# Kernel tuning notes

Measured on AMD Instinct MI355X. Metric: run time of the kernel, lower is better.

## Reference

```python
import jax, jax.numpy as jnp
import numpy as np

D_MODEL, D_FF, N_EXPERTS, TOP_K = 1024, 4096, 8, 2
B, S = 4, 1024
EPS = 1e-5

def setup_inputs() -> dict:
    key = jax.random.key(0)
    ks = jax.random.split(key, 8)
    sd = 1.0 / np.sqrt(D_MODEL)
    sf = 1.0 / np.sqrt(D_FF)
    return {
        "x": jax.random.normal(ks[0], (B, S, D_MODEL), dtype=jnp.float32),
        "mask": jnp.ones((B, S), dtype=bool),
        "Wg": jax.random.normal(ks[1], (D_MODEL, N_EXPERTS), dtype=jnp.float32) * sd,
        "W1": jax.random.normal(ks[2], (N_EXPERTS, D_MODEL, D_FF), dtype=jnp.float32) * sd,
        "b1": jnp.zeros((N_EXPERTS, D_FF), dtype=jnp.float32),
        "W2": jax.random.normal(ks[3], (N_EXPERTS, D_FF, D_MODEL), dtype=jnp.float32) * sf,
        "b2": jnp.zeros((N_EXPERTS, D_MODEL), dtype=jnp.float32),
        "gamma": jnp.ones((D_MODEL,), dtype=jnp.float32),
        "beta": jnp.zeros((D_MODEL,), dtype=jnp.float32),
    }

def _layernorm(x, gamma, beta):
    mu = jnp.mean(x, axis=-1, keepdims=True)
    var = jnp.mean(jnp.square(x - mu), axis=-1, keepdims=True)
    return (x - mu) * jax.lax.rsqrt(var + EPS) * gamma + beta

def reference(x, mask, Wg, W1, b1, W2, b2, gamma, beta):
    Bq, Sq, D = x.shape
    T = Bq * Sq
    xf = x.reshape(T, D)                       # [T, D]
    logits = xf @ Wg                           # [T, E]
    probs = jax.nn.softmax(logits, axis=-1)
    topv, topi = jax.lax.top_k(probs, TOP_K)   # [T, K]
    w = topv / jnp.sum(topv, axis=-1, keepdims=True)
    combine = jnp.zeros((T, N_EXPERTS), dtype=probs.dtype)
    combine = combine.at[jnp.arange(T)[:, None], topi].add(w)  # [T, E]
    # all-expert FFN (dense reference for grouped expert GEMMs)
    h = jax.nn.relu(jnp.einsum('td,edf->tef', xf, W1) + b1)    # [T, E, F]
    ye = jnp.einsum('tef,efd->ted', h, W2) + b2                # [T, E, D]
    y = jnp.einsum('te,ted->td', combine, ye)                  # [T, D]
    # load-balancing aux loss (Switch-style)
    frac_tokens = jnp.mean((combine > 0).astype(probs.dtype), axis=0)  # [E]
    frac_probs = jnp.mean(probs, axis=0)                                # [E]
    aux_loss = N_EXPERTS * jnp.sum(frac_tokens * frac_probs)
    out = _layernorm(x + y.reshape(Bq, Sq, D), gamma, beta)
    return out, aux_loss
```

## Files before the change

### kernel.cpp

```cpp
#include <hip/hip_runtime.h>
#include <cstdint>
#include <cstddef>


#define T_TOK 4096
#define DM 1024
#define DF 4096
#define NE 8
#define CAP 9216
#define MAXMT 72

typedef __bf16 bf16;
typedef __bf16 bf16x4 __attribute__((ext_vector_type(4)));
typedef __bf16 bf16x8 __attribute__((ext_vector_type(8)));
typedef float f32x4 __attribute__((ext_vector_type(4)));

struct Meta {
  int pad_off[NE + 1];
  int n_mtiles;
  int tile_e[80];
  int tile_m0[80];
};

__global__ __launch_bounds__(256) void router_kernel(
    const float* __restrict__ x, const float* __restrict__ Wg,
    int* __restrict__ topi, float* __restrict__ topw, float* __restrict__ probs) {
  int wave = threadIdx.x >> 6, lane = threadIdx.x & 63;
  int t = blockIdx.x * 4 + wave;
  const float* xr = x + (size_t)t * DM;
  float acc[NE];
#pragma unroll
  for (int e = 0; e < NE; e++) acc[e] = 0.f;
  for (int d0 = 0; d0 < DM; d0 += 64) {
    float xv = xr[d0 + lane];
    const float4* wrow = (const float4*)(Wg + (size_t)(d0 + lane) * NE);
    float4 w0 = wrow[0], w1 = wrow[1];
    acc[0] += xv * w0.x; acc[1] += xv * w0.y; acc[2] += xv * w0.z; acc[3] += xv * w0.w;
    acc[4] += xv * w1.x; acc[5] += xv * w1.y; acc[6] += xv * w1.z; acc[7] += xv * w1.w;
  }
#pragma unroll
  for (int off = 32; off >= 1; off >>= 1) {
#pragma unroll
    for (int e = 0; e < NE; e++) acc[e] += __shfl_xor(acc[e], off);
  }
  if (lane == 0) {
    float m = acc[0];
#pragma unroll
    for (int e = 1; e < NE; e++) m = fmaxf(m, acc[e]);
    float p[NE], s = 0.f;
#pragma unroll
    for (int e = 0; e < NE; e++) { p[e] = expf(acc[e] - m); s += p[e]; }
    float inv = 1.f / s;
#pragma unroll
    for (int e = 0; e < NE; e++) { p[e] *= inv; probs[t * NE + e] = p[e]; }
    int i1 = 0; float v1 = acc[0];
#pragma unroll
    for (int e = 1; e < NE; e++) if (acc[e] > v1) { v1 = acc[e]; i1 = e; }
    int i2 = -1; float v2 = -1e30f;
#pragma unroll
    for (int e = 0; e < NE; e++) if (e != i1 && acc[e] > v2) { v2 = acc[e]; i2 = e; }
    float sw = p[i1] + p[i2];
    topi[t * 2] = i1; topi[t * 2 + 1] = i2;
    topw[t * 2] = p[i1] / sw; topw[t * 2 + 1] = p[i2] / sw;
  }
}

__global__ __launch_bounds__(256) void prep_kernel(
    const int* __restrict__ topi, const float* __restrict__ probs,
    Meta* __restrict__ meta, float* __restrict__ aux_out) {
  __shared__ int scnt[NE];
  __shared__ float wps[4][NE];
  int tid = threadIdx.x, lane = tid & 63, wave = tid >> 6;
  if (tid < NE) scnt[tid] = 0;
  __syncthreads();
  for (int i = tid; i < T_TOK * 2; i += 256) atomicAdd(&scnt[topi[i]], 1);
  float lp[NE];
#pragma unroll
  for (int e = 0; e < NE; e++) lp[e] = 0.f;
  for (int tt = tid; tt < T_TOK; tt += 256) {
#pragma unroll
    for (int e = 0; e < NE; e++) lp[e] += probs[tt * NE + e];
  }
#pragma unroll
  for (int off = 32; off >= 1; off >>= 1) {
#pragma unroll
    for (int e = 0; e < NE; e++) lp[e] += __shfl_xor(lp[e], off);
  }
  if (lane == 0) {
#pragma unroll
    for (int e = 0; e < NE; e++) wps[wave][e] = lp[e];
  }
  __syncthreads();
  if (tid == 0) {
    float aux = 0.f;
    int nt = 0, po = 0;
    for (int e = 0; e < NE; e++) {
      float ps = wps[0][e] + wps[1][e] + wps[2][e] + wps[3][e];
      aux += (float)scnt[e] * ps;
      meta->pad_off[e] = po;
      int pc = (scnt[e] + 127) & ~127;
      for (int i = 0; i < pc / 128; i++) {
        meta->tile_e[nt] = e; meta->tile_m0[nt] = po + i * 128; nt++;
      }
      po += pc;
    }
    meta->pad_off[NE] = po;
    meta->n_mtiles = nt;
    aux_out[0] = aux * (8.f / ((float)T_TOK * (float)T_TOK));
  }
}

__global__ __launch_bounds__(64) void scatter_kernel(
    const int* __restrict__ topi, const float* __restrict__ topw,
    const Meta* __restrict__ meta,
    int* __restrict__ t_of, float* __restrict__ w_of, int* __restrict__ k_of) {
  int e = blockIdx.x, lane = threadIdx.x;
  int base = meta->pad_off[e];
  for (int c = 0; c < T_TOK * 2; c += 64) {
    int idx = c + lane;
    int sel = (topi[idx] == e) ? 1 : 0;
    unsigned long long mask = __ballot(sel);
    if (sel) {
      int rank = __popcll(mask & ((1ull << lane) - 1ull));
      int s = base + rank;
      t_of[s] = idx >> 1;
      k_of[s] = idx & 1;
      w_of[s] = topw[idx];
    }
    base += (int)__popcll(mask);
  }
}

__global__ __launch_bounds__(256) void gather_kernel(
    const float* __restrict__ x, const int* __restrict__ t_of,
    unsigned short* __restrict__ Xg_u) {
  int s = blockIdx.x;
  int t = t_of[s];
  if (t < 0) return;
  bf16* Xg = (bf16*)Xg_u;
  int i = threadIdx.x;
  float4 v = ((const float4*)(x + (size_t)t * DM))[i];
  bf16x4 o = {(bf16)v.x, (bf16)v.y, (bf16)v.z, (bf16)v.w};
  ((bf16x4*)(Xg + (size_t)s * DM))[i] = o;
}

__global__ __launch_bounds__(256) void transpose_kernel(
    const float* __restrict__ src, unsigned short* __restrict__ dst_u, int R, int C) {
  bf16* dst = (bf16*)dst_u;
  int e = blockIdx.z;
  int c0 = blockIdx.x * 32, r0 = blockIdx.y * 32;
  int tx = threadIdx.x & 31, ty = threadIdx.x >> 5;
  __shared__ float tile[32][33];
  const float* s = src + (size_t)e * R * C;
#pragma unroll
  for (int j = 0; j < 32; j += 8)
    tile[ty + j][tx] = s[(size_t)(r0 + ty + j) * C + c0 + tx];
  __syncthreads();
  bf16* d = dst + (size_t)e * C * R;
#pragma unroll
  for (int j = 0; j < 32; j += 8)
    d[(size_t)(c0 + ty + j) * R + r0 + tx] = (bf16)tile[tx][ty + j];
}

__device__ inline void gl_lds16(const void* g, void* l) {
  __builtin_amdgcn_global_load_lds(
      (const __attribute__((address_space(1))) unsigned int*)g,
      (__attribute__((address_space(3))) unsigned int*)l, 16, 0, 0);
}

template <int MODE>
__global__ __launch_bounds__(256) void gemm_kernel(
    const unsigned short* __restrict__ A_u, const unsigned short* __restrict__ Bt_u,
    const float* __restrict__ bias, const Meta* __restrict__ meta,
    int K, int N,
    unsigned short* __restrict__ Hout_u, float* __restrict__ Yout,
    const int* __restrict__ t_of, const int* __restrict__ k_of,
    const float* __restrict__ w_of) {
  int bx = blockIdx.x;
  if (bx >= meta->n_mtiles) return;
  const bf16* A = (const bf16*)A_u;
  const bf16* Bt = (const bf16*)Bt_u;
  int e = meta->tile_e[bx];
  int m0 = meta->tile_m0[bx];
  int n0 = blockIdx.y * 128;
  const bf16* Be = Bt + (size_t)e * N * K;

  __shared__ bf16 As[128 * 64];
  __shared__ bf16 Bs[128 * 64];

  int tid = threadIdx.x, lane = tid & 63, wave = tid >> 6;
  int wr = wave >> 1, wc = wave & 1;
  int srow = lane >> 3;
  int scol = (lane & 7) * 8;

  const bf16* Ag = A + (size_t)(m0 + wave * 8 + srow) * K + scol;
  const bf16* Bg = Be + (size_t)(n0 + wave * 8 + srow) * K + scol;
  bf16* AsW = As + wave * 512;
  bf16* BsW = Bs + wave * 512;

  f32x4 acc[4][4];
#pragma unroll
  for (int i = 0; i < 4; i++)
#pragma unroll
    for (int j = 0; j < 4; j++) acc[i][j] = (f32x4){0.f, 0.f, 0.f, 0.f};

  int fr = lane & 15;
  int kq = (lane >> 4) * 8;

  for (int k0 = 0; k0 < K; k0 += 64) {
#pragma unroll
    for (int r = 0; r < 4; r++) {
      gl_lds16(Ag + (size_t)(r * 32) * K + k0, AsW + r * 2048);
      gl_lds16(Bg + (size_t)(r * 32) * K + k0, BsW + r * 2048);
    }
    __syncthreads();
#pragma unroll
    for (int kk = 0; kk < 64; kk += 32) {
      bf16x8 af[4], bfr[4];
#pragma unroll
      for (int i = 0; i < 4; i++)
        af[i] = *(const bf16x8*)&As[(wr * 64 + i * 16 + fr) * 64 + kk + kq];
#pragma unroll
      for (int j = 0; j < 4; j++)
        bfr[j] = *(const bf16x8*)&Bs[(wc * 64 + j * 16 + fr) * 64 + kk + kq];
#pragma unroll
      for (int i = 0; i < 4; i++)
#pragma unroll
        for (int j = 0; j < 4; j++)
          acc[i][j] = __builtin_amdgcn_mfma_f32_16x16x32_bf16(af[i], bfr[j], acc[i][j], 0, 0, 0);
    }
    __syncthreads();
  }

  int crow = (lane >> 4) * 4;
  int ccol = lane & 15;
  if (MODE == 1) {
    bf16* Hout = (bf16*)Hout_u;
#pragma unroll
    for (int i = 0; i < 4; i++) {
#pragma unroll
      for (int r = 0; r < 4; r++) {
        int slot = m0 + wr * 64 + i * 16 + crow + r;
        bf16* hrow = Hout + (size_t)slot * N;
#pragma unroll
        for (int j = 0; j < 4; j++) {
          int n = n0 + wc * 64 + j * 16 + ccol;
          float v = acc[i][j][r] + bias[e * N + n];
          hrow[n] = (bf16)fmaxf(v, 0.f);
        }
      }
    }
  } else {
#pragma unroll
    for (int i = 0; i < 4; i++) {
#pragma unroll
      for (int r = 0; r < 4; r++) {
        int slot = m0 + wr * 64 + i * 16 + crow + r;
        int t = t_of[slot];
        if (t < 0) continue;
        int ks = k_of[slot];
        float w = w_of[slot];
        float* yrow = Yout + ((size_t)ks * T_TOK + t) * DM;
#pragma unroll
        for (int j = 0; j < 4; j++) {
          int n = n0 + wc * 64 + j * 16 + ccol;
          yrow[n] = (acc[i][j][r] + bias[e * DM + n]) * w;
        }
      }
    }
  }
}

__global__ __launch_bounds__(256) void ln_kernel(
    const float* __restrict__ x, const float* __restrict__ Ysl,
    const float* __restrict__ gamma, const float* __restrict__ beta,
    float* __restrict__ out) {
  int t = blockIdx.x, tid = threadIdx.x, lane = tid & 63, wave = tid >> 6;
  float4 a = ((const float4*)(x + (size_t)t * DM))[tid];
  float4 y0 = ((const float4*)(Ysl + (size_t)t * DM))[tid];
  float4 y1 = ((const float4*)(Ysl + ((size_t)T_TOK + t) * DM))[tid];
  float4 sv;
  sv.x = a.x + y0.x + y1.x; sv.y = a.y + y0.y + y1.y;
  sv.z = a.z + y0.z + y1.z; sv.w = a.w + y0.w + y1.w;
  float sum = sv.x + sv.y + sv.z + sv.w;
  float sq = sv.x * sv.x + sv.y * sv.y + sv.z * sv.z + sv.w * sv.w;
#pragma unroll
  for (int off = 32; off >= 1; off >>= 1) {
    sum += __shfl_xor(sum, off);
    sq += __shfl_xor(sq, off);
  }
  __shared__ float ls[4], lq[4], stats[2];
  if (lane == 0) { ls[wave] = sum; lq[wave] = sq; }
  __syncthreads();
  if (tid == 0) {
    float ts = ls[0] + ls[1] + ls[2] + ls[3];
    float tq = lq[0] + lq[1] + lq[2] + lq[3];
    float mu = ts * (1.f / DM);
    float var = tq * (1.f / DM) - mu * mu;
    stats[0] = mu;
    stats[1] = rsqrtf(var + 1e-5f);
  }
  __syncthreads();
  float mu = stats[0], rs = stats[1];
  float4 g = ((const float4*)gamma)[tid];
  float4 b = ((const float4*)beta)[tid];
  float4 o;
  o.x = (sv.x - mu) * rs * g.x + b.x;
  o.y = (sv.y - mu) * rs * g.y + b.y;
  o.z = (sv.z - mu) * rs * g.z + b.z;
  o.w = (sv.w - mu) * rs * g.w + b.w;
  ((float4*)(out + (size_t)t * DM))[tid] = o;
}

extern "C" void kernel_launch(void* const* d_in, const int* in_sizes, int n_in,
                              void* d_out, int out_size, void* d_ws, size_t ws_size,
                              hipStream_t stream) {
  const float* x     = (const float*)d_in[0];
  const float* Wg    = (const float*)d_in[2];
  const float* W1    = (const float*)d_in[3];
  const float* b1    = (const float*)d_in[4];
  const float* W2    = (const float*)d_in[5];
  const float* b2    = (const float*)d_in[6];
  const float* gamma = (const float*)d_in[7];
  const float* beta  = (const float*)d_in[8];
  float* out = (float*)d_out;

  char* ws = (char*)d_ws;
  size_t off = 0;
  auto alloc = [&](size_t bytes) -> void* {
    off = (off + 4095) & ~(size_t)4095;
    void* p = ws + off;
    off += bytes;
    return p;
  };
  Meta* meta   = (Meta*)alloc(sizeof(Meta));
  int* topi    = (int*)alloc((size_t)T_TOK * 2 * 4);
  float* topw  = (float*)alloc((size_t)T_TOK * 2 * 4);
  float* probs = (float*)alloc((size_t)T_TOK * NE * 4);
  int* t_of    = (int*)alloc((size_t)CAP * 4);
  int* k_of    = (int*)alloc((size_t)CAP * 4);
  float* w_of  = (float*)alloc((size_t)CAP * 4);
  unsigned short* Xg   = (unsigned short*)alloc((size_t)CAP * DM * 2);
  unsigned short* Hbuf = (unsigned short*)alloc((size_t)CAP * DF * 2);
  float* Ysl           = (float*)alloc((size_t)2 * T_TOK * DM * 4);
  unsigned short* WT   = (unsigned short*)alloc((size_t)NE * DM * DF * 2);

  hipMemsetAsync(t_of, 0xFF, (size_t)CAP * 4, stream);

  router_kernel<<<dim3(T_TOK / 4), dim3(256), 0, stream>>>(x, Wg, topi, topw, probs);
  prep_kernel<<<dim3(1), dim3(256), 0, stream>>>(topi, probs, meta, out + (size_t)T_TOK * DM);
  scatter_kernel<<<dim3(NE), dim3(64), 0, stream>>>(topi, topw, meta, t_of, w_of, k_of);
  gather_kernel<<<dim3(CAP), dim3(256), 0, stream>>>(x, t_of, Xg);

  transpose_kernel<<<dim3(DF / 32, DM / 32, NE), dim3(256), 0, stream>>>(W1, WT, DM, DF);
  gemm_kernel<1><<<dim3(MAXMT, DF / 128), dim3(256), 0, stream>>>(
      Xg, WT, b1, meta, DM, DF, Hbuf, (float*)nullptr,
      (const int*)nullptr, (const int*)nullptr, (const float*)nullptr);

  transpose_kernel<<<dim3(DM / 32, DF / 32, NE), dim3(256), 0, stream>>>(W2, WT, DF, DM);
  gemm_kernel<2><<<dim3(MAXMT, DM / 128), dim3(256), 0, stream>>>(
      Hbuf, WT, b2, meta, DF, DM, (unsigned short*)nullptr, Ysl, t_of, k_of, w_of);

  ln_kernel<<<dim3(T_TOK), dim3(256), 0, stream>>>(x, Ysl, gamma, beta, out);
}
```

Measured before the change: 751.1 us.

## Split-K second expert GEMM, swizzle LDS tiles, vectorize transpose stores

The second expert GEMM now splits K in two over a new grid z dimension. Each half writes its partial sums to a separate buffer, one of which reuses the Xg region, and the layernorm kernel adds the four partial slices. Both GEMMs also XOR-swizzle the 16-byte granules in LDS, both on global-to-LDS load and on fragment read, to cut bank conflicts. The weight transpose writes bf16 pairs instead of single elements. The split doubles the parallelism of the narrow N=1024 GEMM at the cost of extra fp32 partial-sum traffic to write and read back in layernorm.

```diff
diff --git a/kernel.cpp b/kernel.cpp
--- a/kernel.cpp
+++ b/kernel.cpp
@@ -11,6 +11,7 @@
 #define MAXMT 72
 
 typedef __bf16 bf16;
+typedef __bf16 bf16x2 __attribute__((ext_vector_type(2)));
 typedef __bf16 bf16x4 __attribute__((ext_vector_type(4)));
 typedef __bf16 bf16x8 __attribute__((ext_vector_type(8)));
 typedef float f32x4 __attribute__((ext_vector_type(4)));
@@ -157,9 +158,14 @@
     tile[ty + j][tx] = s[(size_t)(r0 + ty + j) * C + c0 + tx];
   __syncthreads();
   bf16* d = dst + (size_t)e * C * R;
-#pragma unroll
-  for (int j = 0; j < 32; j += 8)
-    d[(size_t)(c0 + ty + j) * R + r0 + tx] = (bf16)tile[tx][ty + j];
+  int wr_ = threadIdx.x & 15;
+  int wc_ = threadIdx.x >> 4;
+#pragma unroll
+  for (int j = 0; j < 32; j += 16) {
+    int c = wc_ + j;
+    bf16x2 v = {(bf16)tile[2 * wr_][c], (bf16)tile[2 * wr_ + 1][c]};
+    *(bf16x2*)&d[(size_t)(c0 + c) * R + r0 + 2 * wr_] = v;
+  }
 }
 
 __device__ inline void gl_lds16(const void* g, void* l) {
@@ -172,8 +178,9 @@
 __global__ __launch_bounds__(256) void gemm_kernel(
     const unsigned short* __restrict__ A_u, const unsigned short* __restrict__ Bt_u,
     const float* __restrict__ bias, const Meta* __restrict__ meta,
-    int K, int N,
-    unsigned short* __restrict__ Hout_u, float* __restrict__ Yout,
+    int Ktot, int Ksp, int N,
+    unsigned short* __restrict__ Hout_u,
+    float* __restrict__ P0, float* __restrict__ P1,
     const int* __restrict__ t_of, const int* __restrict__ k_of,
     const float* __restrict__ w_of) {
   int bx = blockIdx.x;
@@ -183,7 +190,8 @@
   int e = meta->tile_e[bx];
   int m0 = meta->tile_m0[bx];
   int n0 = blockIdx.y * 128;
-  const bf16* Be = Bt + (size_t)e * N * K;
+  int koff = blockIdx.z * Ksp;
+  const bf16* Be = Bt + (size_t)e * N * Ktot;
 
   __shared__ bf16 As[128 * 64];
   __shared__ bf16 Bs[128 * 64];
@@ -191,10 +199,11 @@
   int tid = threadIdx.x, lane = tid & 63, wave = tid >> 6;
   int wr = wave >> 1, wc = wave & 1;
   int srow = lane >> 3;
-  int scol = (lane & 7) * 8;
-
-  const bf16* Ag = A + (size_t)(m0 + wave * 8 + srow) * K + scol;
-  const bf16* Bg = Be + (size_t)(n0 + wave * 8 + srow) * K + scol;
+  int sgran = lane & 7;
+  int gcol = (sgran ^ srow) * 8;
+
+  const bf16* Ag = A + (size_t)(m0 + wave * 8 + srow) * Ktot + koff + gcol;
+  const bf16* Bg = Be + (size_t)(n0 + wave * 8 + srow) * Ktot + koff + gcol;
   bf16* AsW = As + wave * 512;
   bf16* BsW = Bs + wave * 512;
 
@@ -205,24 +214,26 @@
     for (int j = 0; j < 4; j++) acc[i][j] = (f32x4){0.f, 0.f, 0.f, 0.f};
 
   int fr = lane & 15;
-  int kq = (lane >> 4) * 8;
-
-  for (int k0 = 0; k0 < K; k0 += 64) {
+  int qh = lane >> 4;
+  int swz = fr & 7;
+
+  for (int k0 = 0; k0 < Ksp; k0 += 64) {
 #pragma unroll
     for (int r = 0; r < 4; r++) {
-      gl_lds16(Ag + (size_t)(r * 32) * K + k0, AsW + r * 2048);
-      gl_lds16(Bg + (size_t)(r * 32) * K + k0, BsW + r * 2048);
+      gl_lds16(Ag + (size_t)(r * 32) * Ktot + k0, AsW + r * 2048);
+      gl_lds16(Bg + (size_t)(r * 32) * Ktot + k0, BsW + r * 2048);
     }
     __syncthreads();
 #pragma unroll
     for (int kk = 0; kk < 64; kk += 32) {
+      int col = (((kk >> 3) | qh) ^ swz) * 8;
       bf16x8 af[4], bfr[4];
 #pragma unroll
       for (int i = 0; i < 4; i++)
-        af[i] = *(const bf16x8*)&As[(wr * 64 + i * 16 + fr) * 64 + kk + kq];
+        af[i] = *(const bf16x8*)&As[(wr * 64 + i * 16 + fr) * 64 + col];
 #pragma unroll
       for (int j = 0; j < 4; j++)
-        bfr[j] = *(const bf16x8*)&Bs[(wc * 64 + j * 16 + fr) * 64 + kk + kq];
+        bfr[j] = *(const bf16x8*)&Bs[(wc * 64 + j * 16 + fr) * 64 + col];
 #pragma unroll
       for (int i = 0; i < 4; i++)
 #pragma unroll
@@ -251,6 +262,8 @@
       }
     }
   } else {
+    float* Pz = (blockIdx.z == 0) ? P0 : P1;
+    int addb = (blockIdx.z == 0) ? 1 : 0;
 #pragma unroll
     for (int i = 0; i < 4; i++) {
 #pragma unroll
@@ -260,11 +273,12 @@
         if (t < 0) continue;
         int ks = k_of[slot];
         float w = w_of[slot];
-        float* yrow = Yout + ((size_t)ks * T_TOK + t) * DM;
+        float* yrow = Pz + ((size_t)ks * T_TOK + t) * DM;
 #pragma unroll
         for (int j = 0; j < 4; j++) {
           int n = n0 + wc * 64 + j * 16 + ccol;
-          yrow[n] = (acc[i][j][r] + bias[e * DM + n]) * w;
+          float bv = addb ? bias[e * DM + n] : 0.f;
+          yrow[n] = (acc[i][j][r] + bv) * w;
         }
       }
     }
@@ -272,16 +286,23 @@
 }
 
 __global__ __launch_bounds__(256) void ln_kernel(
-    const float* __restrict__ x, const float* __restrict__ Ysl,
+    const float* __restrict__ x,
+    const float* __restrict__ P0, const float* __restrict__ P1,
     const float* __restrict__ gamma, const float* __restrict__ beta,
     float* __restrict__ out) {
   int t = blockIdx.x, tid = threadIdx.x, lane = tid & 63, wave = tid >> 6;
-  float4 a = ((const float4*)(x + (size_t)t * DM))[tid];
-  float4 y0 = ((const float4*)(Ysl + (size_t)t * DM))[tid];
-  float4 y1 = ((const float4*)(Ysl + ((size_t)T_TOK + t) * DM))[tid];
+  size_t row = (size_t)t * DM;
+  size_t kstride = (size_t)T_TOK * DM;
+  float4 a  = ((const float4*)(x + row))[tid];
+  float4 y0 = ((const float4*)(P0 + row))[tid];
+  float4 y1 = ((const float4*)(P0 + kstride + row))[tid];
+  float4 y2 = ((const float4*)(P1 + row))[tid];
+  float4 y3 = ((const float4*)(P1 + kstride + row))[tid];
   float4 sv;
-  sv.x = a.x + y0.x + y1.x; sv.y = a.y + y0.y + y1.y;
-  sv.z = a.z + y0.z + y1.z; sv.w = a.w + y0.w + y1.w;
+  sv.x = a.x + y0.x + y1.x + y2.x + y3.x;
+  sv.y = a.y + y0.y + y1.y + y2.y + y3.y;
+  sv.z = a.z + y0.z + y1.z + y2.z + y3.z;
+  sv.w = a.w + y0.w + y1.w + y2.w + y3.w;
   float sum = sv.x + sv.y + sv.z + sv.w;
   float sq = sv.x * sv.x + sv.y * sv.y + sv.z * sv.z + sv.w * sv.w;
 #pragma unroll
@@ -309,7 +330,7 @@
   o.y = (sv.y - mu) * rs * g.y + b.y;
   o.z = (sv.z - mu) * rs * g.z + b.z;
   o.w = (sv.w - mu) * rs * g.w + b.w;
-  ((float4*)(out + (size_t)t * DM))[tid] = o;
+  ((float4*)(out + row))[tid] = o;
 }
 
 extern "C" void kernel_launch(void* const* d_in, const int* in_sizes, int n_in,
@@ -340,9 +361,13 @@
   int* t_of    = (int*)alloc((size_t)CAP * 4);
   int* k_of    = (int*)alloc((size_t)CAP * 4);
   float* w_of  = (float*)alloc((size_t)CAP * 4);
-  unsigned short* Xg   = (unsigned short*)alloc((size_t)CAP * DM * 2);
+  size_t xg_bytes = (size_t)CAP * DM * 2;
+  size_t p_bytes  = (size_t)2 * T_TOK * DM * 4;
+  char* xg_region = (char*)alloc(xg_bytes > p_bytes ? xg_bytes : p_bytes);
+  unsigned short* Xg = (unsigned short*)xg_region;
+  float* Psp1        = (float*)xg_region;
   unsigned short* Hbuf = (unsigned short*)alloc((size_t)CAP * DF * 2);
-  float* Ysl           = (float*)alloc((size_t)2 * T_TOK * DM * 4);
+  float* Psp0          = (float*)alloc(p_bytes);
   unsigned short* WT   = (unsigned short*)alloc((size_t)NE * DM * DF * 2);
 
   hipMemsetAsync(t_of, 0xFF, (size_t)CAP * 4, stream);
@@ -353,13 +378,14 @@
   gather_kernel<<<dim3(CAP), dim3(256), 0, stream>>>(x, t_of, Xg);
 
   transpose_kernel<<<dim3(DF / 32, DM / 32, NE), dim3(256), 0, stream>>>(W1, WT, DM, DF);
-  gemm_kernel<1><<<dim3(MAXMT, DF / 128), dim3(256), 0, stream>>>(
-      Xg, WT, b1, meta, DM, DF, Hbuf, (float*)nullptr,
+  gemm_kernel<1><<<dim3(MAXMT, DF / 128, 1), dim3(256), 0, stream>>>(
+      Xg, WT, b1, meta, DM, DM, DF, Hbuf, (float*)nullptr, (float*)nullptr,
       (const int*)nullptr, (const int*)nullptr, (const float*)nullptr);
 
   transpose_kernel<<<dim3(DM / 32, DF / 32, NE), dim3(256), 0, stream>>>(W2, WT, DF, DM);
-  gemm_kernel<2><<<dim3(MAXMT, DM / 128), dim3(256), 0, stream>>>(
-      Hbuf, WT, b2, meta, DF, DM, (unsigned short*)nullptr, Ysl, t_of, k_of, w_of);
-
-  ln_kernel<<<dim3(T_TOK), dim3(256), 0, stream>>>(x, Ysl, gamma, beta, out);
-}
+  gemm_kernel<2><<<dim3(MAXMT, DM / 128, 2), dim3(256), 0, stream>>>(
+      Hbuf, WT, b2, meta, DF, DF / 2, DM, (unsigned short*)nullptr, Psp0, Psp1,
+      t_of, k_of, w_of);
+
+  ln_kernel<<<dim3(T_TOK), dim3(256), 0, stream>>>(x, Psp0, Psp1, gamma, beta, out);
+}
```

After: 674.6 us. -10.2%, faster.
